# Kernel tuning notes

Hardware: AMD Instinct MI355X
Metric: run time of the kernel (lower is better)

## Reference

```python
import jax, jax.numpy as jnp
import numpy as np


def setup_inputs() -> dict:
    key = jax.random.key(0)
    k1, k2 = jax.random.split(key)
    N, D, n_bags, per_bag = 8192, 512, 64, 128
    features = jax.random.normal(k1, (N, D), dtype=jnp.float32)
    # sorted bag indicator: 64 bags x 128 instances each
    batch = jnp.repeat(jnp.arange(n_bags, dtype=jnp.int32), per_bag)
    W = jax.random.normal(k2, (D, D), dtype=jnp.float32) * np.float32(1.0 / np.sqrt(D))
    b = jnp.zeros((D,), dtype=jnp.float32)
    return {"features": features, "W": W, "b": b, "batch": batch, "n_topk": 16, "n_bags": n_bags}


def reference(features, W, b, batch, n_topk, n_bags):
    N = features.shape[0]
    # F.normalize(dim=1): x / max(||x||, eps)
    norm = jnp.sqrt(jnp.sum(features * features, axis=1, keepdims=True))
    nf = features / jnp.maximum(norm, 1e-12)
    corr = nf @ nf.T  # [N, N] cosine-similarity map
    same_bag = batch[:, None] == batch[None, :]
    adj = jnp.where(same_bag, corr, 0.0)
    # scatter-zero the (N - n_topk) smallest per row == keep n_topk largest per row
    _, top_idx = jax.lax.top_k(adj, n_topk)  # [N, n_topk]
    keep = jnp.zeros((N, N), dtype=bool).at[jnp.arange(N)[:, None], top_idx].set(True)
    adj = jnp.where(keep, adj, 0.0)
    # dense_to_sparse()[0] keeps only indices -> unit edge weights for GCNConv.
    # GCNConv (gcn_norm, add_self_loops=True): A_hat = binarized adjacency with diag forced to 1.
    eye = jnp.eye(N, dtype=bool)
    A = jnp.where(eye, 1.0, (adj != 0).astype(features.dtype))  # [N, N]
    deg = jnp.sum(A, axis=0)  # degree scattered on target (col) index in PyG
    dis = jax.lax.rsqrt(deg)  # deg >= 1 thanks to self loops
    xw = features @ W  # [N, D]
    # out[col] = d[col]^-1/2 * sum_row A[row,col] * d[row]^-1/2 * xw[row]
    gcn_out = dis[:, None] * (A.T @ (dis[:, None] * xw)) + b
    # one-hot^T @ features == per-bag segment sum
    agg = jax.ops.segment_sum(gcn_out, batch, num_segments=n_bags)  # [n_bags, D]
    return agg, adj
```

## Files before the change

kernel.cpp:

```cpp
#include <hip/hip_runtime.h>
#include <hip/hip_bf16.h>

#define N 8192
#define D 512
#define NBAGS 64
#define PER_BAG 128
#define TOPK 16

#define WS_INVN   0
#define WS_SIM    32768
#define WS_KIDX   4227072
#define WS_KCNT   4751360
#define WS_DEG    4784128
#define WS_FW     4816896

__global__ void norm_kernel(const float* __restrict__ feat,
                            float* __restrict__ invn,
                            int* __restrict__ deg) {
    int t = threadIdx.x;
    if (blockIdx.x < 32) deg[blockIdx.x * 256 + t] = 0;
    int lane = t & 63, w = t >> 6;
    int r = blockIdx.x * 4 + w;
    const float4* fr = (const float4*)(feat + (size_t)r * D);
    float4 a = fr[lane];
    float4 bq = fr[lane + 64];
    float ss = a.x * a.x + a.y * a.y + a.z * a.z + a.w * a.w
             + bq.x * bq.x + bq.y * bq.y + bq.z * bq.z + bq.w * bq.w;
    #pragma unroll
    for (int off = 32; off > 0; off >>= 1) ss += __shfl_down(ss, off);
    if (lane == 0) invn[r] = 1.0f / fmaxf(sqrtf(ss), 1e-12f);
}

#define KC 32
__global__ void sim_kernel(const float* __restrict__ feat,
                           const float* __restrict__ invn,
                           float* __restrict__ sim) {
    int rg = blockIdx.x;
    int bag = blockIdx.y;
    int t = threadIdx.x;
    __shared__ float colT[KC][132];
    __shared__ float rowT[KC][36];
    int bagBase = bag * PER_BAG;
    int rowBase = bagBase + rg * 32;
    int tx = t & 31;
    int ty = t >> 5;
    float4 acc[4] = {{0,0,0,0},{0,0,0,0},{0,0,0,0},{0,0,0,0}};

    int kk = t & 31;
    int sub = t >> 5;
    for (int k0 = 0; k0 < D; k0 += KC) {
        __syncthreads();
        #pragma unroll
        for (int c0 = 0; c0 < 16; ++c0) {
            int c = sub * 16 + c0;
            colT[kk][c] = feat[(size_t)(bagBase + c) * D + k0 + kk];
        }
        #pragma unroll
        for (int r0 = 0; r0 < 4; ++r0) {
            int r = sub * 4 + r0;
            rowT[kk][r] = feat[(size_t)(rowBase + r) * D + k0 + kk];
        }
        __syncthreads();
        #pragma unroll
        for (int k = 0; k < KC; ++k) {
            float4 cv = *(const float4*)&colT[k][4 * tx];
            float4 rv = *(const float4*)&rowT[k][4 * ty];
            acc[0].x += rv.x * cv.x; acc[0].y += rv.x * cv.y;
            acc[0].z += rv.x * cv.z; acc[0].w += rv.x * cv.w;
            acc[1].x += rv.y * cv.x; acc[1].y += rv.y * cv.y;
            acc[1].z += rv.y * cv.z; acc[1].w += rv.y * cv.w;
            acc[2].x += rv.z * cv.x; acc[2].y += rv.z * cv.y;
            acc[2].z += rv.z * cv.z; acc[2].w += rv.z * cv.w;
            acc[3].x += rv.w * cv.x; acc[3].y += rv.w * cv.y;
            acc[3].z += rv.w * cv.z; acc[3].w += rv.w * cv.w;
        }
    }
    float ic0 = invn[bagBase + 4 * tx];
    float ic1 = invn[bagBase + 4 * tx + 1];
    float ic2 = invn[bagBase + 4 * tx + 2];
    float ic3 = invn[bagBase + 4 * tx + 3];
    #pragma unroll
    for (int i = 0; i < 4; ++i) {
        int gr = rowBase + 4 * ty + i;
        float ir = invn[gr];
        float4 o = { acc[i].x * ir * ic0, acc[i].y * ir * ic1,
                     acc[i].z * ir * ic2, acc[i].w * ir * ic3 };
        *(float4*)&sim[(size_t)gr * PER_BAG + 4 * tx] = o;
    }
}

__global__ void topk_fill_kernel(const float* __restrict__ sim,
                                 float* __restrict__ adjOut,
                                 int* __restrict__ keptIdx,
                                 int* __restrict__ keptCnt,
                                 int* __restrict__ deg) {
    int r = blockIdx.x;
    int t = threadIdx.x;
    int bag = r >> 7;
    int rl = r & 127;
    int bagBase = bag << 7;
    __shared__ float rowv[PER_BAG];
    rowv[t] = 0.0f;
    rowv[t + 64] = 0.0f;
    const float* srow = sim + (size_t)r * PER_BAG;
    float o0 = srow[t], o1 = srow[t + 64];
    float v0 = o0, v1 = o1;
    int cnt = 0;
    bool p0 = false, p1 = false;

    #pragma unroll 1
    for (int it = 0; it < TOPK; ++it) {
        float bv; int bi;
        if (v0 >= v1) { bv = v0; bi = t; } else { bv = v1; bi = t + 64; }
        #pragma unroll
        for (int s = 1; s < 64; s <<= 1) {
            float ov = __shfl_xor(bv, s);
            int oi = __shfl_xor(bi, s);
            if (ov > bv || (ov == bv && oi < bi)) { bv = ov; bi = oi; }
        }
        if (bv <= 0.0f) break;
        if (t == 0) keptIdx[(size_t)r * TOPK + cnt] = bi;
        cnt++;
        if (bi == t)            { rowv[t] = o0;      v0 = -1e30f; p0 = true; }
        else if (bi == t + 64)  { rowv[t + 64] = o1; v1 = -1e30f; p1 = true; }
    }
    if (t == 0) keptCnt[r] = cnt;
    if (p0) atomicAdd(&deg[bagBase + t], 1);
    if (p1) atomicAdd(&deg[bagBase + t + 64], 1);
    if (t == (rl & 63)) {
        bool selfPicked = (rl < 64) ? p0 : p1;
        if (!selfPicked) atomicAdd(&deg[r], 1);
    }

    float4* rowp = (float4*)(adjOut + (size_t)r * N);
    int winLo = bag * 32;
    #pragma unroll
    for (int i = 0; i < 32; ++i) {
        int f = t + i * 64;
        float4 val = {0.0f, 0.0f, 0.0f, 0.0f};
        if (f >= winLo && f < winLo + 32)
            val = *(const float4*)&rowv[(f - winLo) * 4];
        rowp[f] = val;
    }
}

__global__ void wfw_kernel(const float* __restrict__ feat,
                           const int* __restrict__ keptIdx,
                           const int* __restrict__ keptCnt,
                           const int* __restrict__ deg,
                           float* __restrict__ FW) {
    int bag = blockIdx.x;
    int chunk = blockIdx.y;
    int t = threadIdx.x;
    __shared__ float wsh[PER_BAG];
    int bagBase = bag * PER_BAG;
    if (t < PER_BAG) {
        int r = bagBase + t;
        int cnt = keptCnt[r];
        float sum = 0.0f;
        bool selfin = false;
        for (int k = 0; k < cnt; ++k) {
            int c = keptIdx[(size_t)r * TOPK + k];
            if (c == t) selfin = true;
            sum += 1.0f / sqrtf((float)deg[bagBase + c]);
        }
        float disr = 1.0f / sqrtf((float)deg[r]);
        if (!selfin) sum += disr;
        wsh[t] = disr * sum;
    }
    __syncthreads();
    int d = chunk * 256 + t;
    float acc = 0.0f;
    #pragma unroll 4
    for (int r = 0; r < PER_BAG; ++r)
        acc += wsh[r] * feat[(size_t)(bagBase + r) * D + d];
    FW[bag * D + d] = acc;
}

__global__ void agg_kernel(const float* __restrict__ FW,
                           const float* __restrict__ Wm,
                           const float* __restrict__ b,
                           float* __restrict__ aggOut) {
    int bag = blockIdx.x;
    int chunk = blockIdx.y;
    int t = threadIdx.x;
    __shared__ float fws[D];
    fws[t] = FW[bag * D + t];
    fws[256 + t] = FW[bag * D + 256 + t];
    __syncthreads();
    int d = chunk * 256 + t;
    float acc = 0.0f;
    #pragma unroll 4
    for (int k = 0; k < D; ++k)
        acc += fws[k] * Wm[(size_t)k * D + d];
    aggOut[bag * D + d] = acc + 128.0f * b[d];
}

extern "C" void kernel_launch(void* const* d_in, const int* in_sizes, int n_in,
                              void* d_out, int out_size, void* d_ws, size_t ws_size,
                              hipStream_t stream) {
    const float* feat = (const float*)d_in[0];
    const float* Wm   = (const float*)d_in[1];
    const float* b    = (const float*)d_in[2];

    char* ws = (char*)d_ws;
    float* invn   = (float*)(ws + WS_INVN);
    float* sim    = (float*)(ws + WS_SIM);
    int* keptIdx  = (int*)(ws + WS_KIDX);
    int* keptCnt  = (int*)(ws + WS_KCNT);
    int* deg      = (int*)(ws + WS_DEG);
    float* FW     = (float*)(ws + WS_FW);

    float* aggOut = (float*)d_out;
    float* adjOut = (float*)d_out + NBAGS * D;

    norm_kernel<<<N / 4, 256, 0, stream>>>(feat, invn, deg);
    sim_kernel<<<dim3(4, NBAGS), 256, 0, stream>>>(feat, invn, sim);
    topk_fill_kernel<<<N, 64, 0, stream>>>(sim, adjOut, keptIdx, keptCnt, deg);
    wfw_kernel<<<dim3(NBAGS, 2), 256, 0, stream>>>(feat, keptIdx, keptCnt, deg, FW);
    agg_kernel<<<dim3(NBAGS, 2), 256, 0, stream>>>(FW, Wm, b, aggOut);
}
```

Measured before the change: 403.0 us.

## Fuse similarity, top-k, and adjacency fill; merge weighted-sum and aggregation kernels

The per-bag similarity GEMM now does top-k selection on its register accumulators, so the intermediate sim buffer is never written or read back. The 256 MB adjacency zero-fill moves into the same kernel, issued as nontemporal stores interleaved with the GEMM k-loop so the writes overlap compute. The FW and agg kernels are merged into one 512-thread kernel per bag, which removes a launch and the FW round trip. The trade-off is fewer blocks (256) carrying the whole zero-fill, which could limit store bandwidth compared with the previous 8192-block fill.

```diff
diff --git a/kernel.cpp b/kernel.cpp
--- a/kernel.cpp
+++ b/kernel.cpp
@@ -7,12 +7,12 @@
 #define PER_BAG 128
 #define TOPK 16
 
+typedef float vfloat4 __attribute__((ext_vector_type(4)));
+
 #define WS_INVN   0
-#define WS_SIM    32768
-#define WS_KIDX   4227072
-#define WS_KCNT   4751360
-#define WS_DEG    4784128
-#define WS_FW     4816896
+#define WS_KIDX   32768
+#define WS_KCNT   557056
+#define WS_DEG    589824
 
 __global__ void norm_kernel(const float* __restrict__ feat,
                             float* __restrict__ invn,
@@ -31,24 +31,36 @@
     if (lane == 0) invn[r] = 1.0f / fmaxf(sqrtf(ss), 1e-12f);
 }
 
-#define KC 32
-__global__ void sim_kernel(const float* __restrict__ feat,
-                           const float* __restrict__ invn,
-                           float* __restrict__ sim) {
+__global__ __launch_bounds__(256, 1) void simtopk_kernel(
+        const float* __restrict__ feat,
+        const float* __restrict__ invn,
+        float* __restrict__ adjOut,
+        int* __restrict__ keptIdx,
+        int* __restrict__ keptCnt,
+        int* __restrict__ deg) {
     int rg = blockIdx.x;
     int bag = blockIdx.y;
     int t = threadIdx.x;
-    __shared__ float colT[KC][132];
-    __shared__ float rowT[KC][36];
+    __shared__ float colT[32][132];
+    __shared__ float rowT[32][36];
     int bagBase = bag * PER_BAG;
     int rowBase = bagBase + rg * 32;
     int tx = t & 31;
     int ty = t >> 5;
-    float4 acc[4] = {{0,0,0,0},{0,0,0,0},{0,0,0,0},{0,0,0,0}};
+    float4 acc[4];
+    #pragma unroll
+    for (int i = 0; i < 4; ++i) acc[i] = make_float4(0.f, 0.f, 0.f, 0.f);
 
     int kk = t & 31;
     int sub = t >> 5;
-    for (int k0 = 0; k0 < D; k0 += KC) {
+    int zrh = t >> 7;
+    int zc  = t & 127;
+    int jw  = bag >> 2;
+    int winLo = bag * 32, winHi = winLo + 32;
+    vfloat4 zf4 = {0.f, 0.f, 0.f, 0.f};
+
+    for (int it = 0; it < 16; ++it) {
+        int k0 = it * 32;
         __syncthreads();
         #pragma unroll
         for (int c0 = 0; c0 < 16; ++c0) {
@@ -61,8 +73,22 @@
             rowT[kk][r] = feat[(size_t)(rowBase + r) * D + k0 + kk];
         }
         __syncthreads();
+        {
+            int zr = 2 * it + zrh;
+            vfloat4* rowp = (vfloat4*)(adjOut + (size_t)(rowBase + zr) * N);
+            #pragma unroll
+            for (int j = 0; j < 16; ++j) {
+                int f = zc + 128 * j;
+                if (j == jw) {
+                    if (f < winLo || f >= winHi)
+                        __builtin_nontemporal_store(zf4, &rowp[f]);
+                } else {
+                    __builtin_nontemporal_store(zf4, &rowp[f]);
+                }
+            }
+        }
         #pragma unroll
-        for (int k = 0; k < KC; ++k) {
+        for (int k = 0; k < 32; ++k) {
             float4 cv = *(const float4*)&colT[k][4 * tx];
             float4 rv = *(const float4*)&rowT[k][4 * ty];
             acc[0].x += rv.x * cv.x; acc[0].y += rv.x * cv.y;
@@ -81,78 +107,68 @@
     float ic3 = invn[bagBase + 4 * tx + 3];
     #pragma unroll
     for (int i = 0; i < 4; ++i) {
-        int gr = rowBase + 4 * ty + i;
-        float ir = invn[gr];
-        float4 o = { acc[i].x * ir * ic0, acc[i].y * ir * ic1,
-                     acc[i].z * ir * ic2, acc[i].w * ir * ic3 };
-        *(float4*)&sim[(size_t)gr * PER_BAG + 4 * tx] = o;
-    }
-}
-
-__global__ void topk_fill_kernel(const float* __restrict__ sim,
-                                 float* __restrict__ adjOut,
-                                 int* __restrict__ keptIdx,
-                                 int* __restrict__ keptCnt,
-                                 int* __restrict__ deg) {
-    int r = blockIdx.x;
-    int t = threadIdx.x;
-    int bag = r >> 7;
-    int rl = r & 127;
-    int bagBase = bag << 7;
-    __shared__ float rowv[PER_BAG];
-    rowv[t] = 0.0f;
-    rowv[t + 64] = 0.0f;
-    const float* srow = sim + (size_t)r * PER_BAG;
-    float o0 = srow[t], o1 = srow[t + 64];
-    float v0 = o0, v1 = o1;
-    int cnt = 0;
-    bool p0 = false, p1 = false;
-
-    #pragma unroll 1
-    for (int it = 0; it < TOPK; ++it) {
-        float bv; int bi;
-        if (v0 >= v1) { bv = v0; bi = t; } else { bv = v1; bi = t + 64; }
-        #pragma unroll
-        for (int s = 1; s < 64; s <<= 1) {
-            float ov = __shfl_xor(bv, s);
-            int oi = __shfl_xor(bi, s);
-            if (ov > bv || (ov == bv && oi < bi)) { bv = ov; bi = oi; }
-        }
-        if (bv <= 0.0f) break;
-        if (t == 0) keptIdx[(size_t)r * TOPK + cnt] = bi;
-        cnt++;
-        if (bi == t)            { rowv[t] = o0;      v0 = -1e30f; p0 = true; }
-        else if (bi == t + 64)  { rowv[t + 64] = o1; v1 = -1e30f; p1 = true; }
-    }
-    if (t == 0) keptCnt[r] = cnt;
-    if (p0) atomicAdd(&deg[bagBase + t], 1);
-    if (p1) atomicAdd(&deg[bagBase + t + 64], 1);
-    if (t == (rl & 63)) {
-        bool selfPicked = (rl < 64) ? p0 : p1;
-        if (!selfPicked) atomicAdd(&deg[r], 1);
-    }
-
-    float4* rowp = (float4*)(adjOut + (size_t)r * N);
-    int winLo = bag * 32;
-    #pragma unroll
-    for (int i = 0; i < 32; ++i) {
-        int f = t + i * 64;
-        float4 val = {0.0f, 0.0f, 0.0f, 0.0f};
-        if (f >= winLo && f < winLo + 32)
-            val = *(const float4*)&rowv[(f - winLo) * 4];
-        rowp[f] = val;
-    }
-}
-
-__global__ void wfw_kernel(const float* __restrict__ feat,
-                           const int* __restrict__ keptIdx,
-                           const int* __restrict__ keptCnt,
-                           const int* __restrict__ deg,
-                           float* __restrict__ FW) {
+        float ir = invn[rowBase + 4 * ty + i];
+        acc[i].x *= ir * ic0; acc[i].y *= ir * ic1;
+        acc[i].z *= ir * ic2; acc[i].w *= ir * ic3;
+    }
+    #pragma unroll
+    for (int i = 0; i < 4; ++i) {
+        int r = rowBase + 4 * ty + i;
+        float o0 = acc[i].x, o1 = acc[i].y, o2 = acc[i].z, o3 = acc[i].w;
+        float w0 = o0, w1 = o1, w2 = o2, w3 = o3;
+        int pm = 0, cnt = 0;
+        #pragma unroll 1
+        for (int itk = 0; itk < TOPK; ++itk) {
+            float bv = w0; int bj = 0;
+            if (w1 > bv) { bv = w1; bj = 1; }
+            if (w2 > bv) { bv = w2; bj = 2; }
+            if (w3 > bv) { bv = w3; bj = 3; }
+            int bi = 4 * tx + bj;
+            #pragma unroll
+            for (int s = 1; s < 32; s <<= 1) {
+                float ov = __shfl_xor(bv, s);
+                int oi = __shfl_xor(bi, s);
+                if (ov > bv || (ov == bv && oi < bi)) { bv = ov; bi = oi; }
+            }
+            if (bv <= 0.0f) break;
+            if (tx == 0) keptIdx[(size_t)r * TOPK + cnt] = bi;
+            cnt++;
+            if ((bi >> 2) == tx) {
+                pm |= 1 << (bi & 3);
+                int q = bi & 3;
+                if (q == 0) w0 = -1e30f;
+                else if (q == 1) w1 = -1e30f;
+                else if (q == 2) w2 = -1e30f;
+                else w3 = -1e30f;
+            }
+        }
+        if (tx == 0) keptCnt[r] = cnt;
+        float4 ov4 = make_float4((pm & 1) ? o0 : 0.0f,
+                                 (pm & 2) ? o1 : 0.0f,
+                                 (pm & 4) ? o2 : 0.0f,
+                                 (pm & 8) ? o3 : 0.0f);
+        *(float4*)(adjOut + (size_t)r * N + bagBase + 4 * tx) = ov4;
+        if (pm & 1) atomicAdd(&deg[bagBase + 4 * tx], 1);
+        if (pm & 2) atomicAdd(&deg[bagBase + 4 * tx + 1], 1);
+        if (pm & 4) atomicAdd(&deg[bagBase + 4 * tx + 2], 1);
+        if (pm & 8) atomicAdd(&deg[bagBase + 4 * tx + 3], 1);
+        int selfCol = rg * 32 + 4 * ty + i;
+        if (tx == (selfCol >> 2) && !((pm >> (selfCol & 3)) & 1))
+            atomicAdd(&deg[bagBase + selfCol], 1);
+    }
+}
+
+__global__ void wfwagg_kernel(const float* __restrict__ feat,
+                              const int* __restrict__ keptIdx,
+                              const int* __restrict__ keptCnt,
+                              const int* __restrict__ deg,
+                              const float* __restrict__ Wm,
+                              const float* __restrict__ b,
+                              float* __restrict__ aggOut) {
     int bag = blockIdx.x;
-    int chunk = blockIdx.y;
     int t = threadIdx.x;
     __shared__ float wsh[PER_BAG];
+    __shared__ float fws[D];
     int bagBase = bag * PER_BAG;
     if (t < PER_BAG) {
         int r = bagBase + t;
@@ -162,38 +178,24 @@
         for (int k = 0; k < cnt; ++k) {
             int c = keptIdx[(size_t)r * TOPK + k];
             if (c == t) selfin = true;
-            sum += 1.0f / sqrtf((float)deg[bagBase + c]);
-        }
-        float disr = 1.0f / sqrtf((float)deg[r]);
+            sum += rsqrtf((float)deg[bagBase + c]);
+        }
+        float disr = rsqrtf((float)deg[r]);
         if (!selfin) sum += disr;
         wsh[t] = disr * sum;
     }
     __syncthreads();
-    int d = chunk * 256 + t;
     float acc = 0.0f;
-    #pragma unroll 4
+    #pragma unroll 8
     for (int r = 0; r < PER_BAG; ++r)
-        acc += wsh[r] * feat[(size_t)(bagBase + r) * D + d];
-    FW[bag * D + d] = acc;
-}
-
-__global__ void agg_kernel(const float* __restrict__ FW,
-                           const float* __restrict__ Wm,
-                           const float* __restrict__ b,
-                           float* __restrict__ aggOut) {
-    int bag = blockIdx.x;
-    int chunk = blockIdx.y;
-    int t = threadIdx.x;
-    __shared__ float fws[D];
-    fws[t] = FW[bag * D + t];
-    fws[256 + t] = FW[bag * D + 256 + t];
+        acc += wsh[r] * feat[(size_t)(bagBase + r) * D + t];
+    fws[t] = acc;
     __syncthreads();
-    int d = chunk * 256 + t;
-    float acc = 0.0f;
-    #pragma unroll 4
+    float acc2 = 0.0f;
+    #pragma unroll 8
     for (int k = 0; k < D; ++k)
-        acc += fws[k] * Wm[(size_t)k * D + d];
-    aggOut[bag * D + d] = acc + 128.0f * b[d];
+        acc2 += fws[k] * Wm[(size_t)k * D + t];
+    aggOut[bag * D + t] = acc2 + 128.0f * b[t];
 }
 
 extern "C" void kernel_launch(void* const* d_in, const int* in_sizes, int n_in,
@@ -205,18 +207,16 @@
 
     char* ws = (char*)d_ws;
     float* invn   = (float*)(ws + WS_INVN);
-    float* sim    = (float*)(ws + WS_SIM);
     int* keptIdx  = (int*)(ws + WS_KIDX);
     int* keptCnt  = (int*)(ws + WS_KCNT);
     int* deg      = (int*)(ws + WS_DEG);
-    float* FW     = (float*)(ws + WS_FW);
 
     float* aggOut = (float*)d_out;
     float* adjOut = (float*)d_out + NBAGS * D;
 
     norm_kernel<<<N / 4, 256, 0, stream>>>(feat, invn, deg);
-    sim_kernel<<<dim3(4, NBAGS), 256, 0, stream>>>(feat, invn, sim);
-    topk_fill_kernel<<<N, 64, 0, stream>>>(sim, adjOut, keptIdx, keptCnt, deg);
-    wfw_kernel<<<dim3(NBAGS, 2), 256, 0, stream>>>(feat, keptIdx, keptCnt, deg, FW);
-    agg_kernel<<<dim3(NBAGS, 2), 256, 0, stream>>>(FW, Wm, b, aggOut);
-}
+    simtopk_kernel<<<dim3(4, NBAGS), 256, 0, stream>>>(feat, invn, adjOut,
+                                                       keptIdx, keptCnt, deg);
+    wfwagg_kernel<<<NBAGS, 512, 0, stream>>>(feat, keptIdx, keptCnt, deg,
+                                             Wm, b, aggOut);
+}
```

After: 367.5 us. 8.8% less time.
